# Kernel tuning notes

Measured on AMD Instinct MI355X. Metric: run time of the kernel, lower is better.

Reference implementation:

```python
import jax, jax.numpy as jnp
import numpy as np

HIDDEN = 64
OUT = 16
NEG = 1e12


def sinusoidal_pos(seq_len, dim, dtype=jnp.float32):
    # kexue.fm SinusoidalPositionEmbedding, merge_mode='zero': [1, S, dim]
    pos = jnp.arange(seq_len, dtype=dtype)[:, None]            # [S,1]
    idx = jnp.arange(dim // 2, dtype=dtype)
    inv_freq = jnp.power(10000.0, -2.0 * idx / dim)            # [dim/2]
    ang = pos * inv_freq[None, :]                              # [S, dim/2]
    emb = jnp.stack([jnp.sin(ang), jnp.cos(ang)], axis=-1)     # [S, dim/2, 2]
    return emb.reshape(seq_len, dim)[None]                     # [1, S, dim]; ::2 = sin, 1::2 = cos


def rotate_half_interleaved(x):
    # result[...,2i] = -x[...,2i+1]; result[...,2i+1] = x[...,2i]
    return jnp.stack([-x[..., 1::2], x[..., ::2]], axis=-1).reshape(x.shape)


def setup_inputs() -> dict:
    key = jax.random.key(0)
    ks = jax.random.split(key, 5)
    B, S, D = 4, 1024, 768
    inputs = jax.random.normal(ks[0], (B, S, D), dtype=jnp.float32)
    mask = jnp.ones((B, S), dtype=jnp.float32)
    W1 = jax.random.normal(ks[1], (D, 2 * HIDDEN), dtype=jnp.float32) * 0.02
    b1 = jax.random.normal(ks[2], (2 * HIDDEN,), dtype=jnp.float32) * 0.02
    W2 = jax.random.normal(ks[3], (2 * HIDDEN, 2 * OUT), dtype=jnp.float32) * 0.02
    b2 = jax.random.normal(ks[4], (2 * OUT,), dtype=jnp.float32) * 0.02
    return {"inputs": inputs, "mask": mask, "W1": W1, "b1": b1, "W2": W2, "b2": b2}


def reference(inputs, mask, W1, b1, W2, b2):
    B, S, _ = inputs.shape
    h = inputs @ W1 + b1                       # [B,S,2H]
    qw, kw = h[..., ::2], h[..., 1::2]         # [B,S,H] each

    pos = sinusoidal_pos(S, HIDDEN, h.dtype)   # [1,S,H]
    cos_pos = jnp.tile(pos[..., 1::2], (1, 1, 2))   # .repeat(1,1,2) tiles, not interleaves
    sin_pos = jnp.tile(pos[..., ::2], (1, 1, 2))
    qw = qw * cos_pos + rotate_half_interleaved(qw) * sin_pos
    kw = kw * cos_pos + rotate_half_interleaved(kw) * sin_pos

    logits = jnp.einsum('bmd,bnd->bmn', qw, kw) / jnp.sqrt(jnp.asarray(HIDDEN, h.dtype))
    bias = jnp.einsum('bnh->bhn', h @ W2 + b2) / 2.0        # [B,2*OUT,S]
    logits = logits[:, None] + bias[:, ::2, None, :] + bias[:, 1::2, :, None]  # [B,OUT,S,S]

    pad = mask[:, None, None, :]                            # broadcast over heads and query dim
    pad = jnp.broadcast_to(pad, (B, OUT, S, S))
    logits = logits * pad - (1.0 - pad) * NEG

    tril = jnp.tril(jnp.ones((S, S), dtype=logits.dtype), -1)
    logits = logits - tril * NEG
    return logits
```

## Files before the change

### kernel.cpp

```cpp
#include <hip/hip_runtime.h>
#include <math.h>

#define NEGV 1000000000000.0f
#define LDSTR 68

__global__ __launch_bounds__(256) void k1_fused(
    const float* __restrict__ x,
    const float* __restrict__ W1,
    const float* __restrict__ b1,
    const float* __restrict__ W2,
    const float* __restrict__ b2,
    float* __restrict__ qw,
    float* __restrict__ kw,
    float* __restrict__ bias)
{
    __shared__ float xs[16][772];
    __shared__ float hs[16][132];
    const int t    = threadIdx.x;
    const int row0 = blockIdx.x * 16;

    {
        const float4* xg = (const float4*)(x + (size_t)row0 * 768);
        #pragma unroll
        for (int it = 0; it < 12; ++it) {
            const int idx = t + it * 256;
            const int r = idx / 192, c4 = idx - r * 192;
            const float4 v = xg[idx];
            *(float4*)&xs[r][c4 * 4] = v;
        }
    }
    __syncthreads();

    const int jc = (t & 31) * 4;
    const int rg = (t >> 5) * 2;
    float accA[4] = {0.f,0.f,0.f,0.f};
    float accB[4] = {0.f,0.f,0.f,0.f};
    #pragma unroll 2
    for (int k = 0; k < 768; k += 4) {
        const float4 xa = *(const float4*)&xs[rg][k];
        const float4 xb = *(const float4*)&xs[rg + 1][k];
        const float xav[4] = {xa.x, xa.y, xa.z, xa.w};
        const float xbv[4] = {xb.x, xb.y, xb.z, xb.w};
        #pragma unroll
        for (int kk = 0; kk < 4; ++kk) {
            const float4 w = *(const float4*)&W1[(size_t)(k + kk) * 128 + jc];
            const float wv[4] = {w.x, w.y, w.z, w.w};
            #pragma unroll
            for (int c = 0; c < 4; ++c) {
                accA[c] = fmaf(xav[kk], wv[c], accA[c]);
                accB[c] = fmaf(xbv[kk], wv[c], accB[c]);
            }
        }
    }
    {
        const float4 bv = *(const float4*)&b1[jc];
        const float bvv[4] = {bv.x, bv.y, bv.z, bv.w};
        #pragma unroll
        for (int c = 0; c < 4; ++c) {
            hs[rg][jc + c]     = accA[c] + bvv[c];
            hs[rg + 1][jc + c] = accB[c] + bvv[c];
        }
    }
    __syncthreads();

    for (int idx = t; idx < 16 * 64; idx += 256) {
        const int r = idx >> 6, c = idx & 63;
        const int rowg = row0 + r;
        const int s = rowg & 1023;
        const int f = c & 31;
        const float invf = exp2f(-0.4152410118609203f * (float)f);
        const float ang = (float)s * invf;
        float sn, cs;
        sincosf(ang, &sn, &cs);
        const int   pc  = (c & 1) ? (c - 1) : (c + 1);
        const float sgn = (c & 1) ? sn : -sn;
        const float qv = fmaf(hs[r][2*c],     cs, hs[r][2*pc]     * sgn);
        const float kv = fmaf(hs[r][2*c + 1], cs, hs[r][2*pc + 1] * sgn);
        qw[(size_t)rowg * 64 + c] = qv;
        kw[(size_t)rowg * 64 + c] = kv;
    }

    for (int idx = t; idx < 16 * 32; idx += 256) {
        const int r = idx >> 5, c = idx & 31;
        const int rowg = row0 + r;
        const int s = rowg & 1023, bb = rowg >> 10;
        float a = 0.f;
        #pragma unroll 4
        for (int k = 0; k < 128; ++k)
            a = fmaf(hs[r][k], W2[k * 32 + c], a);
        bias[(size_t)(bb * 32 + c) * 1024 + s] = (a + b2[c]) * 0.5f;
    }
}

__global__ __launch_bounds__(256) void k2_outer(
    const float* __restrict__ qw, const float* __restrict__ kw,
    const float* __restrict__ bias, const float* __restrict__ mask,
    float* __restrict__ out)
{
    __shared__ float qs[64 * LDSTR];
    __shared__ float ks[64 * LDSTR];
    __shared__ float bA[16][64];
    __shared__ float bB[16][64];
    __shared__ float padv[64];

    const int t  = threadIdx.x;
    const int n0 = blockIdx.x * 64;
    const int m0 = blockIdx.y * 64;
    const int b  = blockIdx.z;

    const float4* qg = (const float4*)(qw + (size_t)(b * 1024 + m0) * 64);
    const float4* kg = (const float4*)(kw + (size_t)(b * 1024 + n0) * 64);
    #pragma unroll
    for (int it = 0; it < 4; ++it) {
        const int idx = t + it * 256;
        const int m = idx >> 4, kgp = idx & 15;
        float4 v = qg[idx];
        qs[(4*kgp + 0) * LDSTR + m] = v.x;
        qs[(4*kgp + 1) * LDSTR + m] = v.y;
        qs[(4*kgp + 2) * LDSTR + m] = v.z;
        qs[(4*kgp + 3) * LDSTR + m] = v.w;
        v = kg[idx];
        ks[(4*kgp + 0) * LDSTR + m] = v.x;
        ks[(4*kgp + 1) * LDSTR + m] = v.y;
        ks[(4*kgp + 2) * LDSTR + m] = v.z;
        ks[(4*kgp + 3) * LDSTR + m] = v.w;
    }
    for (int idx = t; idx < 16 * 64; idx += 256) {
        const int o = idx >> 6, c = idx & 63;
        bA[o][c] = bias[(size_t)(b * 32 + 2*o)     * 1024 + n0 + c];
        bB[o][c] = bias[(size_t)(b * 32 + 2*o + 1) * 1024 + m0 + c];
    }
    if (t < 64) padv[t] = mask[b * 1024 + n0 + t];
    __syncthreads();

    const int tn = t & 15, tm = t >> 4;
    float acc[4][4];
    #pragma unroll
    for (int i = 0; i < 4; ++i)
        #pragma unroll
        for (int c = 0; c < 4; ++c) acc[i][c] = 0.f;

    #pragma unroll 8
    for (int k = 0; k < 64; ++k) {
        const float4 qv = *(const float4*)&qs[k * LDSTR + 4 * tm];
        const float4 kv = *(const float4*)&ks[k * LDSTR + 4 * tn];
        const float qa[4] = {qv.x, qv.y, qv.z, qv.w};
        const float ka[4] = {kv.x, kv.y, kv.z, kv.w};
        #pragma unroll
        for (int i = 0; i < 4; ++i)
            #pragma unroll
            for (int c = 0; c < 4; ++c)
                acc[i][c] = fmaf(qa[i], ka[c], acc[i][c]);
    }

    const float4 pv = *(const float4*)&padv[4 * tn];
    const float p[4] = {pv.x, pv.y, pv.z, pv.w};
    float negterm[4];
    #pragma unroll
    for (int c = 0; c < 4; ++c) negterm[c] = (1.f - p[c]) * NEGV;
    const int ng = n0 + 4 * tn;

    #pragma unroll
    for (int o = 0; o < 16; ++o) {
        const float4 av = *(const float4*)&bA[o][4 * tn];
        const float a[4] = {av.x, av.y, av.z, av.w};
        #pragma unroll
        for (int i = 0; i < 4; ++i) {
            const int mg = m0 + 4 * tm + i;
            const float vb = bB[o][4 * tm + i];
            float rv[4];
            #pragma unroll
            for (int c = 0; c < 4; ++c) {
                float v = fmaf(acc[i][c], 0.125f, a[c] + vb);
                v = v * p[c] - negterm[c];
                if (ng + c < mg) v -= NEGV;
                rv[c] = v;
            }
            float4 r4; r4.x = rv[0]; r4.y = rv[1]; r4.z = rv[2]; r4.w = rv[3];
            *(float4*)(out + ((size_t)((b * 16 + o) * 1024 + mg)) * 1024 + ng) = r4;
        }
    }
}

extern "C" void kernel_launch(void* const* d_in, const int* in_sizes, int n_in,
                              void* d_out, int out_size, void* d_ws, size_t ws_size,
                              hipStream_t stream) {
    const float* x    = (const float*)d_in[0];
    const float* mask = (const float*)d_in[1];
    const float* W1   = (const float*)d_in[2];
    const float* b1   = (const float*)d_in[3];
    const float* W2   = (const float*)d_in[4];
    const float* b2   = (const float*)d_in[5];
    float* out = (float*)d_out;

    float* ws   = (float*)d_ws;
    float* qw   = ws;
    float* kw   = ws + 4096 * 64;
    float* bias = ws + 2 * 4096 * 64;

    hipLaunchKernelGGL(k1_fused, dim3(256), dim3(256), 0, stream,
                       x, W1, b1, W2, b2, qw, kw, bias);
    hipLaunchKernelGGL(k2_outer, dim3(16, 16, 4), dim3(256), 0, stream,
                       qw, kw, bias, mask, out);
}
```

Baseline: 359.0 us.

## Split outer kernel into QK score pass and coalesced streaming broadcast kernel

The fused outer kernel is split in two. The first computes the masked, causal-penalised QK scores once per batch into a workspace buffer. The second streams that buffer with one row segment per wavefront, adding the per-head biases and writing the 16 head outputs with fully coalesced float4 stores. The premultiplied column bias (bias times mask) is now produced in the first kernel. This removes the repeated per-head epilogue arithmetic and the strided output writes, at the cost of an extra 16 MB score round-trip through memory and one more launch.

```diff
diff --git a/kernel.cpp b/kernel.cpp
--- a/kernel.cpp
+++ b/kernel.cpp
@@ -6,13 +6,15 @@
 
 __global__ __launch_bounds__(256) void k1_fused(
     const float* __restrict__ x,
+    const float* __restrict__ mask,
     const float* __restrict__ W1,
     const float* __restrict__ b1,
     const float* __restrict__ W2,
     const float* __restrict__ b2,
     float* __restrict__ qw,
     float* __restrict__ kw,
-    float* __restrict__ bias)
+    float* __restrict__ bias,
+    float* __restrict__ bAp)
 {
     __shared__ float xs[16][772];
     __shared__ float hs[16][132];
@@ -88,19 +90,19 @@
         #pragma unroll 4
         for (int k = 0; k < 128; ++k)
             a = fmaf(hs[r][k], W2[k * 32 + c], a);
-        bias[(size_t)(bb * 32 + c) * 1024 + s] = (a + b2[c]) * 0.5f;
-    }
-}
-
-__global__ __launch_bounds__(256) void k2_outer(
+        const float v = (a + b2[c]) * 0.5f;
+        bias[(size_t)(bb * 32 + c) * 1024 + s] = v;
+        if ((c & 1) == 0)
+            bAp[(size_t)(bb * 16 + (c >> 1)) * 1024 + s] = v * mask[bb * 1024 + s];
+    }
+}
+
+__global__ __launch_bounds__(256) void k2a_qk(
     const float* __restrict__ qw, const float* __restrict__ kw,
-    const float* __restrict__ bias, const float* __restrict__ mask,
-    float* __restrict__ out)
+    const float* __restrict__ mask, float* __restrict__ Sc)
 {
     __shared__ float qs[64 * LDSTR];
     __shared__ float ks[64 * LDSTR];
-    __shared__ float bA[16][64];
-    __shared__ float bB[16][64];
     __shared__ float padv[64];
 
     const int t  = threadIdx.x;
@@ -125,11 +127,6 @@
         ks[(4*kgp + 2) * LDSTR + m] = v.z;
         ks[(4*kgp + 3) * LDSTR + m] = v.w;
     }
-    for (int idx = t; idx < 16 * 64; idx += 256) {
-        const int o = idx >> 6, c = idx & 63;
-        bA[o][c] = bias[(size_t)(b * 32 + 2*o)     * 1024 + n0 + c];
-        bB[o][c] = bias[(size_t)(b * 32 + 2*o + 1) * 1024 + m0 + c];
-    }
     if (t < 64) padv[t] = mask[b * 1024 + n0 + t];
     __syncthreads();
 
@@ -155,29 +152,54 @@
 
     const float4 pv = *(const float4*)&padv[4 * tn];
     const float p[4] = {pv.x, pv.y, pv.z, pv.w};
-    float negterm[4];
-    #pragma unroll
-    for (int c = 0; c < 4; ++c) negterm[c] = (1.f - p[c]) * NEGV;
     const int ng = n0 + 4 * tn;
 
     #pragma unroll
-    for (int o = 0; o < 16; ++o) {
-        const float4 av = *(const float4*)&bA[o][4 * tn];
-        const float a[4] = {av.x, av.y, av.z, av.w};
-        #pragma unroll
-        for (int i = 0; i < 4; ++i) {
-            const int mg = m0 + 4 * tm + i;
-            const float vb = bB[o][4 * tm + i];
-            float rv[4];
-            #pragma unroll
-            for (int c = 0; c < 4; ++c) {
-                float v = fmaf(acc[i][c], 0.125f, a[c] + vb);
-                v = v * p[c] - negterm[c];
-                if (ng + c < mg) v -= NEGV;
-                rv[c] = v;
-            }
-            float4 r4; r4.x = rv[0]; r4.y = rv[1]; r4.z = rv[2]; r4.w = rv[3];
-            *(float4*)(out + ((size_t)((b * 16 + o) * 1024 + mg)) * 1024 + ng) = r4;
+    for (int i = 0; i < 4; ++i) {
+        const int mg = m0 + 4 * tm + i;
+        float4 s4;
+        float rv[4];
+        #pragma unroll
+        for (int c = 0; c < 4; ++c) {
+            float kadd = (p[c] - 1.f) * NEGV;
+            if (ng + c < mg) kadd -= NEGV;
+            rv[c] = fmaf(acc[i][c] * 0.125f, p[c], kadd);
+        }
+        s4.x = rv[0]; s4.y = rv[1]; s4.z = rv[2]; s4.w = rv[3];
+        *(float4*)&Sc[(size_t)(b * 1024 + mg) * 1024 + ng] = s4;
+    }
+}
+
+__global__ __launch_bounds__(256) void k2b_stream(
+    const float* __restrict__ Sc, const float* __restrict__ bias,
+    const float* __restrict__ bAp, const float* __restrict__ mask,
+    float* __restrict__ out)
+{
+    const int t = threadIdx.x;
+    const int l = t & 63;
+    const int W = (blockIdx.x << 2) + (t >> 6);
+
+    #pragma unroll
+    for (int rep = 0; rep < 2; ++rep) {
+        const int Wp = W + rep * 8192;
+        const int b  = Wp >> 12;
+        const int m  = (Wp >> 2) & 1023;
+        const int nq = Wp & 3;
+        const int n4 = nq * 64 + l;
+
+        const float4 sc4 = *(const float4*)&Sc[(size_t)(b * 1024 + m) * 1024 + n4 * 4];
+        const float4 p4  = *(const float4*)&mask[b * 1024 + n4 * 4];
+
+        #pragma unroll
+        for (int o = 0; o < 16; ++o) {
+            const float4 a4 = *(const float4*)&bAp[(size_t)(b * 16 + o) * 1024 + n4 * 4];
+            const float  bo = bias[(size_t)(b * 32 + 2 * o + 1) * 1024 + m];
+            float4 r;
+            r.x = fmaf(bo, p4.x, sc4.x + a4.x);
+            r.y = fmaf(bo, p4.y, sc4.y + a4.y);
+            r.z = fmaf(bo, p4.z, sc4.z + a4.z);
+            r.w = fmaf(bo, p4.w, sc4.w + a4.w);
+            *(float4*)&out[(size_t)((b * 16 + o) * 1024 + m) * 1024 + n4 * 4] = r;
         }
     }
 }
@@ -195,11 +217,15 @@
 
     float* ws   = (float*)d_ws;
     float* qw   = ws;
-    float* kw   = ws + 4096 * 64;
-    float* bias = ws + 2 * 4096 * 64;
+    float* kw   = ws + 262144;
+    float* bias = ws + 524288;
+    float* bAp  = ws + 655360;
+    float* Sc   = ws + 720896;
 
     hipLaunchKernelGGL(k1_fused, dim3(256), dim3(256), 0, stream,
-                       x, W1, b1, W2, b2, qw, kw, bias);
-    hipLaunchKernelGGL(k2_outer, dim3(16, 16, 4), dim3(256), 0, stream,
-                       qw, kw, bias, mask, out);
-}
+                       x, mask, W1, b1, W2, b2, qw, kw, bias, bAp);
+    hipLaunchKernelGGL(k2a_qk, dim3(16, 16, 4), dim3(256), 0, stream,
+                       qw, kw, mask, Sc);
+    hipLaunchKernelGGL(k2b_stream, dim3(2048), dim3(256), 0, stream,
+                       Sc, bias, bAp, mask, out);
+}
```

Measured after the change: 367.8 us. +2.5%, slower.
